# Kernel tuning notes

Measured on AMD Instinct MI355X. Metric: run time of the kernel, lower is better.

## Reference

```python
import jax, jax.numpy as jnp
import numpy as np

DIM = 768
NUM_HEADS = 12
HEAD_DIM = DIM // NUM_HEADS
WS = 14                       # window_size (14, 14)
N_TOK = WS * WS + 1           # 197 (patches + cls)
NUM_REL = (2 * WS - 1) ** 2 + 3  # 732
SCALE = HEAD_DIM ** -0.5


def _build_rel_index():
    # Faithful port of the BEiT relative_position_index construction.
    coords = np.stack(np.meshgrid(np.arange(WS), np.arange(WS), indexing='ij'))  # (2, WS, WS)
    flat = coords.reshape(2, -1)                                   # (2, WS*WS)
    rel = flat[:, :, None] - flat[:, None, :]                      # (2, P, P)
    rel = rel.transpose(1, 2, 0).astype(np.int64)                  # (P, P, 2)
    rel[:, :, 0] += WS - 1
    rel[:, :, 1] += WS - 1
    rel[:, :, 0] *= 2 * WS - 1
    idx = np.zeros((N_TOK, N_TOK), dtype=np.int64)
    idx[1:, 1:] = rel.sum(-1)
    idx[0, :] = NUM_REL - 3
    idx[:, 0] = NUM_REL - 2
    idx[0, 0] = NUM_REL - 1
    return idx


def setup_inputs() -> dict:
    key = jax.random.key(0)
    ks = jax.random.split(key, 7)
    B = 64
    x = jax.random.normal(ks[0], (B, N_TOK, DIM), dtype=jnp.float32)
    qkv_w = jax.random.normal(ks[1], (3 * DIM, DIM), dtype=jnp.float32) * 0.02
    q_bias = jnp.zeros((DIM,), dtype=jnp.float32)
    v_bias = jnp.zeros((DIM,), dtype=jnp.float32)
    rel_table = jax.random.normal(ks[2], (NUM_REL, NUM_HEADS), dtype=jnp.float32) * 0.02
    proj_w = jax.random.normal(ks[3], (DIM, DIM), dtype=jnp.float32) * 0.02
    proj_b = jnp.zeros((DIM,), dtype=jnp.float32)
    rel_index = jnp.asarray(_build_rel_index())  # (N, N) int64
    return {"x": x, "qkv_w": qkv_w, "q_bias": q_bias, "v_bias": v_bias,
            "rel_table": rel_table, "proj_w": proj_w, "proj_b": proj_b,
            "rel_index": rel_index}


def reference(x, qkv_w, q_bias, v_bias, rel_table, proj_w, proj_b, rel_index):
    B, N, C = x.shape
    # qkv bias = concat(q_bias, zeros, v_bias)
    qkv_b = jnp.concatenate([q_bias, jnp.zeros_like(v_bias), v_bias])
    qkv = x @ qkv_w.T + qkv_b                       # (B, N, 3C)
    qkv = qkv.reshape(B, N, 3, NUM_HEADS, HEAD_DIM).transpose(2, 0, 3, 1, 4)
    q, k, v = qkv[0], qkv[1], qkv[2]                # each (B, H, N, hd)
    attn = jnp.einsum('bhqd,bhkd->bhqk', q * SCALE, k)
    # relative position bias gathered from table: (N, N, H) -> (H, N, N)
    bias = rel_table[rel_index].transpose(2, 0, 1)
    attn = attn + bias[None]
    attn = jax.nn.softmax(attn, axis=-1)
    out = jnp.einsum('bhqk,bhkd->bhqd', attn, v)    # (B, H, N, hd)
    out = out.transpose(0, 2, 1, 3).reshape(B, N, -1)
    return out @ proj_w.T + proj_b
```

## Files before the change

### kernel.cpp

```cpp
#include <hip/hip_runtime.h>
#include <stdint.h>

#define NTOK 197
#define HD 64
#define NH 12
#define CDIM 768
#define BB 64
#define MTOT (BB*NTOK)
#define MPAD 12672
#define SCALE 0.125f
#define BTP 208

typedef __attribute__((ext_vector_type(8))) short short8;
typedef __attribute__((ext_vector_type(4))) float f32x4;
typedef unsigned short us;

__device__ __forceinline__ us f2b(float f){
    union { float f; uint32_t u; } v; v.f = f;
    uint32_t u = v.u;
    uint32_t r = u + 0x7fffu + ((u >> 16) & 1u);
    return (us)(r >> 16);
}

__device__ __forceinline__ float b2f(us b){
    union { uint32_t u; float f; } v; v.u = ((uint32_t)b) << 16;
    return v.f;
}

__device__ __forceinline__ void gload16(const us* g, us* l){
    __builtin_amdgcn_global_load_lds((const __attribute__((address_space(1))) void*)g,
                                     (__attribute__((address_space(3))) void*)l, 16, 0, 0);
}

#define LGKM0_BAR() do{ asm volatile("s_waitcnt lgkmcnt(0)" ::: "memory"); \
                        __builtin_amdgcn_s_barrier(); }while(0)

__device__ __forceinline__ void cvt4(const float* in, us* out, int i){
    float4 v = ((const float4*)in)[i];
    ushort4 o;
    o.x = f2b(v.x); o.y = f2b(v.y); o.z = f2b(v.z); o.w = f2b(v.w);
    ((ushort4*)out)[i] = o;
}

__global__ void prep_kernel(const float* __restrict__ x, const float* __restrict__ qkv_w,
                            const float* __restrict__ proj_w,
                            const int* __restrict__ rel_index, const float* __restrict__ rel_table,
                            us* __restrict__ xb, us* __restrict__ wqkv, us* __restrict__ wproj,
                            float* __restrict__ biasT)
{
    const int N1 = MTOT*CDIM/4;
    const int N2 = 3*CDIM*CDIM/4;
    const int N3 = CDIM*CDIM/4;
    const int N4 = BTP*BTP;
    const int total = N1+N2+N3+N4;
    for (int i = blockIdx.x*blockDim.x + threadIdx.x; i < total; i += gridDim.x*blockDim.x){
        if (i < N1) cvt4(x, xb, i);
        else if (i < N1+N2) cvt4(qkv_w, wqkv, i-N1);
        else if (i < N1+N2+N3) cvt4(proj_w, wproj, i-N1-N2);
        else {
            int t = i - N1 - N2 - N3;
            int col = t / BTP, row = t - col*BTP;
            if (row < NTOK && col < NTOK){
                int idx = rel_index[row*NTOK + col];
                #pragma unroll
                for (int h = 0; h < NH; ++h)
                    biasT[((size_t)h*BTP + col)*BTP + row] = rel_table[idx*NH + h];
            } else {
                #pragma unroll
                for (int h = 0; h < NH; ++h)
                    biasT[((size_t)h*BTP + col)*BTP + row] = 0.f;
            }
        }
    }
}

__global__ __launch_bounds__(512,1) void pgemm5_kernel(
    const us* __restrict__ A, const us* __restrict__ Bw,
    us* __restrict__ Qo, us* __restrict__ Ko, us* __restrict__ Vo,
    const float* __restrict__ b0, const float* __restrict__ b2, int ny, int total)
{
    __shared__ __align__(16) us AsB[3][24576];
    us* cbuf = &AsB[2][0];
    const int tid  = threadIdx.x;
    const int lane = tid & 63;
    const int wave = tid >> 6;
    const int wrr = wave >> 2;
    const int wcc = wave & 3;
    const int lr = lane & 15;
    const int g  = lane >> 4;

    const int id  = blockIdx.x;
    const int xcd = id & 7;
    const int jb  = id >> 3;
    const int qs  = total >> 3, rs = total & 7;
    const int Ssp = xcd*qs + (xcd < rs ? xcd : rs);
    const int L   = qs + (xcd < rs ? 1 : 0);
    const int qb  = L >> 5, rb = L & 31;
    const int cnt = qb + (jb < rb ? 1 : 0);
    const int w0  = Ssp + jb*qb + (jb < rb ? jb : rb);
    if (cnt == 0) return;

    int aoff[2], bofs[4];
    int aldo[2], bldo[4];
    #pragma unroll
    for (int p=0;p<2;p++){
        int c = tid + p*512;
        int row = c >> 3, ch = c & 7;
        aoff[p] = row*CDIM + ((ch ^ (row & 7))*8);
        aldo[p] = c*8;
    }
    #pragma unroll
    for (int jj=0;jj<4;jj++){
        int c = tid + jj*512;
        int row = c >> 3, ch = c & 7;
        bofs[jj] = row*CDIM + ((ch ^ (row & 7))*8);
        bldo[jj] = 8192 + c*8;
    }

    const int S = cnt * 12;
    auto stageStep = [&](int x){
        int tt = x / 12, kt = x - tt*12;
        int ww = w0 + tt;
        int bx = ww / ny, by = ww - bx*ny;
        const us* pA = A  + (size_t)(bx*128)*CDIM;
        const us* pB = Bw + (size_t)(by*256)*CDIM;
        int buf = x % 3;
        #pragma unroll
        for (int p=0;p<2;p++) gload16(pA + aoff[p] + kt*64, &AsB[buf][aldo[p]]);
        #pragma unroll
        for (int jj=0;jj<4;jj++) gload16(pB + bofs[jj] + kt*64, &AsB[buf][bldo[jj]]);
    };

    stageStep(0);
    if (S > 1) stageStep(1);
    int s = 0;

    #pragma unroll 1
    for (int tt = 0; tt < cnt; ++tt){
        const int w  = w0 + tt;
        const int bx = w / ny, by = w - bx*ny;
        const int m0 = bx*128, n0 = by*256;
        const int whc = n0 / CDIM;
        float addf[4];
        const float sclf = (whc == 0) ? SCALE : 1.f;
        #pragma unroll
        for (int nt=0;nt<4;nt++){
            int n = n0 + wcc*64 + nt*16 + lr;
            int hn = n - whc*CDIM;
            addf[nt] = (whc == 0) ? b0[hn] : (whc == 2 ? b2[hn] : 0.f);
        }

        f32x4 acc[4][4];
        #pragma unroll
        for (int i=0;i<4;i++)
            #pragma unroll
            for (int jj=0;jj<4;jj++) acc[i][jj] = (f32x4){0.f,0.f,0.f,0.f};

        #pragma unroll 1
        for (int kt = 0; kt < 12; ++kt){
            if (s == S-1) asm volatile("s_waitcnt vmcnt(0)" ::: "memory");
            else          asm volatile("s_waitcnt vmcnt(6)" ::: "memory");
            __builtin_amdgcn_s_barrier();
            if (s + 2 < S) stageStep(s + 2);
            const us* la = &AsB[s % 3][0];
            const us* lb = &AsB[s % 3][8192];
            #pragma unroll
            for (int kk=0; kk<2; ++kk){
                const int co = 8*((kk*4 + g) ^ (lr & 7));
                short8 af[4], bf[4];
                #pragma unroll
                for (int mt=0;mt<4;mt++)
                    af[mt] = *(const short8*)&la[(wrr*64+mt*16+lr)*64 + co];
                #pragma unroll
                for (int nt=0;nt<4;nt++)
                    bf[nt] = *(const short8*)&lb[(wcc*64+nt*16+lr)*64 + co];
                __builtin_amdgcn_s_setprio(1);
                #pragma unroll
                for (int mt=0;mt<4;mt++)
                    #pragma unroll
                    for (int nt=0;nt<4;nt++)
                        acc[mt][nt] = __builtin_amdgcn_mfma_f32_16x16x32_bf16(af[mt], bf[nt], acc[mt][nt], 0,0,0);
                __builtin_amdgcn_s_setprio(0);
            }
            ++s;
        }

        LGKM0_BAR();

        const us* outp = (whc == 0 ? Qo : (whc == 1 ? Ko : Vo));
        #pragma unroll 1
        for (int half = 0; half < 2; ++half){
            if ((wcc >> 1) == half){
                #pragma unroll
                for (int mt=0;mt<4;mt++)
                    #pragma unroll
                    for (int rr=0;rr<4;rr++){
                        int row = wrr*64 + mt*16 + g*4 + rr;
                        #pragma unroll
                        for (int nt=0;nt<4;nt++){
                            int col = (wcc & 1)*64 + nt*16 + lr;
                            cbuf[row*132 + col] = f2b((acc[mt][nt][rr] + addf[nt]) * sclf);
                        }
                    }
            }
            LGKM0_BAR();
            #pragma unroll
            for (int p=0;p<4;p++){
                int c = tid + p*512;
                int row = c >> 4, ch = c & 15;
                int m = m0 + row;
                if (m < MTOT){
                    short8 vv = *(const short8*)&cbuf[row*132 + ch*8];
                    int n = n0 + half*128 + ch*8;
                    int hn = n - whc*CDIM;
                    int h  = hn >> 6, d0 = hn & 63;
                    int bidx = m / NTOK;
                    int tok  = m - bidx*NTOK;
                    size_t off = ((size_t)((bidx*NH + h)*NTOK + tok))*HD + d0;
                    *(short8*)((us*)outp + off) = vv;
                }
            }
            LGKM0_BAR();
        }
    }
}

__global__ __launch_bounds__(256) void proj_gemm_kernel(
    const us* __restrict__ A, const us* __restrict__ Bw,
    float* __restrict__ Cout, const float* __restrict__ b0, int ny)
{
    __shared__ __align__(16) us lds[32768];
    us* As = lds;
    us* Bs = lds + 16384;
    const int tid  = threadIdx.x;
    const int lane = tid & 63;
    const int wave = tid >> 6;
    const int wr = wave >> 1, wc = wave & 1;
    const int lr = lane & 15;
    const int g  = lane >> 4;

    const int NB   = gridDim.x;
    const int base = NB >> 3;
    const int rem  = NB & 7;
    const int id   = blockIdx.x;
    const int xcd  = id & 7;
    const int qq   = id >> 3;
    const int start = (xcd < rem) ? xcd*(base+1) : rem*(base+1) + (xcd-rem)*base;
    const int w    = start + qq;
    const int bx   = w / ny;
    const int by   = w - bx*ny;
    const int m0 = bx * 128;
    const int n0 = by * 128;
    const int NT = CDIM / 128;

    const int row0 = tid >> 4;
    const int cg   = (tid & 15) ^ row0;

    float addf[4];
    #pragma unroll
    for (int nt=0;nt<4;nt++) addf[nt] = b0[n0 + wc*64 + nt*16 + lr];

    f32x4 acc[4][4];
    #pragma unroll
    for (int i=0;i<4;i++)
        #pragma unroll
        for (int j=0;j<4;j++) acc[i][j] = (f32x4){0.f,0.f,0.f,0.f};

    const us* gA = A  + (size_t)(m0 + row0)*CDIM + cg*8;
    const us* gB = Bw + (size_t)(n0 + row0)*CDIM + cg*8;

    #pragma unroll 1
    for (int kt = 0; kt < NT; ++kt){
        __syncthreads();
        #pragma unroll
        for (int j=0;j<8;j++){
            gload16(gA + (size_t)j*16*CDIM + kt*128, As + tid*8 + j*2048);
            gload16(gB + (size_t)j*16*CDIM + kt*128, Bs + tid*8 + j*2048);
        }
        __syncthreads();
        #pragma unroll
        for (int kk=0; kk<4; ++kk){
            const int co = 8*((kk*4 + g) ^ lr);
            short8 af[4], bf[4];
            #pragma unroll
            for (int mt=0;mt<4;mt++)
                af[mt] = *(const short8*)&As[(wr*64+mt*16+lr)*128 + co];
            #pragma unroll
            for (int nt=0;nt<4;nt++)
                bf[nt] = *(const short8*)&Bs[(wc*64+nt*16+lr)*128 + co];
            __builtin_amdgcn_s_setprio(1);
            #pragma unroll
            for (int mt=0;mt<4;mt++)
                #pragma unroll
                for (int nt=0;nt<4;nt++)
                    acc[mt][nt] = __builtin_amdgcn_mfma_f32_16x16x32_bf16(af[mt], bf[nt], acc[mt][nt], 0,0,0);
            __builtin_amdgcn_s_setprio(0);
        }
    }

    __syncthreads();
    #pragma unroll
    for (int mt=0;mt<4;mt++)
        #pragma unroll
        for (int r=0;r<4;r++){
            int row = wr*64 + mt*16 + g*4 + r;
            #pragma unroll
            for (int nt=0;nt<4;nt++){
                int col = wc*64 + nt*16 + lr;
                lds[row*132 + col] = f2b(acc[mt][nt][r] + addf[nt]);
            }
        }
    __syncthreads();
    #pragma unroll
    for (int j=0;j<8;j++){
        int c2  = tid + j*256;
        int row = c2 >> 4;
        int ch  = c2 & 15;
        int m = m0 + row;
        if (m >= MTOT) continue;
        short8 vv = *(const short8*)&lds[row*132 + ch*8];
        int n = n0 + ch*8;
        float4 f0, f1;
        f0.x = b2f((us)vv[0]); f0.y = b2f((us)vv[1]); f0.z = b2f((us)vv[2]); f0.w = b2f((us)vv[3]);
        f1.x = b2f((us)vv[4]); f1.y = b2f((us)vv[5]); f1.z = b2f((us)vv[6]); f1.w = b2f((us)vv[7]);
        *(float4*)&Cout[(size_t)m*CDIM + n]     = f0;
        *(float4*)&Cout[(size_t)m*CDIM + n + 4] = f1;
    }
}

__global__ __launch_bounds__(256) void attn_kernel(
    const us* __restrict__ Q,
    const us* __restrict__ K,
    const us* __restrict__ V,
    const float* __restrict__ biasT,
    us* __restrict__ Ao)
{
    __shared__ us Vt[64][232];
    __shared__ us Ps[4][16][232];
    const int bh = blockIdx.x;
    const int b = bh / NH;
    const int h = bh - b*NH;
    const us* Qh = Q + (size_t)bh*NTOK*HD;
    const us* Kh = K + (size_t)bh*NTOK*HD;
    const us* Vh = V + (size_t)bh*NTOK*HD;
    const float* bT = biasT + (size_t)h*BTP*BTP;
    const int tid = threadIdx.x, lane = tid & 63, wave = tid >> 6;
    const int lr = lane & 15, g = lane >> 4, ko = g*8;

    for (int i = tid; i < 64*232/2; i += 256) ((uint32_t*)Vt)[i] = 0;
    __syncthreads();
    {
        int d0 = (tid & 7) * 8;
        for (int t = tid >> 3; t < NTOK; t += 32){
            short8 v = *(const short8*)&Vh[t*HD + d0];
            #pragma unroll
            for (int j=0;j<8;j++) Vt[d0+j][t] = (us)v[j];
        }
    }
    __syncthreads();

    for (int s = wave; s < 13; s += 4){
        int qrow = s*16 + lr; qrow = qrow > 196 ? 196 : qrow;
        short8 qa0 = *(const short8*)&Qh[qrow*HD + ko];
        short8 qa1 = *(const short8*)&Qh[qrow*HD + 32 + ko];
        f32x4 S[13];
        #pragma unroll
        for (int t=0;t<13;t++){
            int kc = t*16 + lr; kc = kc > 196 ? 196 : kc;
            short8 kb0 = *(const short8*)&Kh[kc*HD + ko];
            short8 kb1 = *(const short8*)&Kh[kc*HD + 32 + ko];
            f32x4 a = (f32x4){0.f,0.f,0.f,0.f};
            a = __builtin_amdgcn_mfma_f32_16x16x32_bf16(qa0, kb0, a, 0,0,0);
            a = __builtin_amdgcn_mfma_f32_16x16x32_bf16(qa1, kb1, a, 0,0,0);
            S[t] = a;
        }
        float rmax[4] = {-3e38f,-3e38f,-3e38f,-3e38f};
        #pragma unroll
        for (int t=0;t<13;t++){
            int col = t*16 + lr;
            bool cok = col < NTOK;
            float4 b4 = *(const float4*)&bT[(size_t)col*BTP + s*16 + g*4];
            #pragma unroll
            for (int r=0;r<4;r++){
                float xv = S[t][r] + ((const float*)&b4)[r];
                xv = cok ? xv : -1e30f;
                S[t][r] = xv;
                rmax[r] = fmaxf(rmax[r], xv);
            }
        }
        #pragma unroll
        for (int r=0;r<4;r++)
            #pragma unroll
            for (int msk=1; msk<16; msk<<=1)
                rmax[r] = fmaxf(rmax[r], __shfl_xor(rmax[r], msk));
        float rsum[4] = {0.f,0.f,0.f,0.f};
        #pragma unroll
        for (int t=0;t<13;t++)
            #pragma unroll
            for (int r=0;r<4;r++){
                float e = __expf(S[t][r] - rmax[r]);
                S[t][r] = e;
                rsum[r] += e;
            }
        #pragma unroll
        for (int r=0;r<4;r++){
            #pragma unroll
            for (int msk=1; msk<16; msk<<=1)
                rsum[r] += __shfl_xor(rsum[r], msk);
            rsum[r] = 1.f / rsum[r];
        }
        #pragma unroll
        for (int t=0;t<13;t++)
            #pragma unroll
            for (int r=0;r<4;r++)
                Ps[wave][g*4+r][t*16+lr] = f2b(S[t][r] * rsum[r]);
        #pragma unroll
        for (int r=0;r<4;r++) Ps[wave][g*4+r][208+lr] = 0;
        asm volatile("s_waitcnt lgkmcnt(0)" ::: "memory");
        f32x4 pv[4];
        #pragma unroll
        for (int nt=0;nt<4;nt++) pv[nt] = (f32x4){0.f,0.f,0.f,0.f};
        #pragma unroll
        for (int ks=0; ks<7; ks++){
            int k0 = ks*32 + ko;
            short8 pa = *(const short8*)&Ps[wave][lr][k0];
            #pragma unroll
            for (int nt=0;nt<4;nt++){
                short8 vb = *(const short8*)&Vt[nt*16+lr][k0];
                pv[nt] = __builtin_amdgcn_mfma_f32_16x16x32_bf16(pa, vb, pv[nt], 0,0,0);
            }
        }
        #pragma unroll
        for (int nt=0;nt<4;nt++)
            #pragma unroll
            for (int r=0;r<4;r++){
                int tok = s*16 + g*4 + r;
                if (tok < NTOK)
                    Ao[(size_t)(b*NTOK + tok)*CDIM + h*HD + nt*16 + lr] = f2b(pv[nt][r]);
            }
    }
}

extern "C" void kernel_launch(void* const* d_in, const int* in_sizes, int n_in,
                              void* d_out, int out_size, void* d_ws, size_t ws_size,
                              hipStream_t stream)
{
    const float* x        = (const float*)d_in[0];
    const float* qkv_w    = (const float*)d_in[1];
    const float* q_bias   = (const float*)d_in[2];
    const float* v_bias   = (const float*)d_in[3];
    const float* rel_tab  = (const float*)d_in[4];
    const float* proj_w   = (const float*)d_in[5];
    const float* proj_b   = (const float*)d_in[6];
    const int*   rel_idx  = (const int*)d_in[7];
    float* out = (float*)d_out;

    char* w = (char*)d_ws;
    us* xb    = (us*)w; w += (size_t)MPAD*CDIM*2;
    us* wqkv  = (us*)w; w += (size_t)3*CDIM*CDIM*2;
    us* wproj = (us*)w; w += (size_t)CDIM*CDIM*2;
    us* Qb    = (us*)w; w += (size_t)BB*NH*NTOK*HD*2;
    us* Kb    = (us*)w; w += (size_t)BB*NH*NTOK*HD*2;
    us* Vb    = (us*)w; w += (size_t)BB*NH*NTOK*HD*2;
    float* biasT = (float*)w; w += (size_t)NH*BTP*BTP*4;
    us* aob   = (us*)w; w += (size_t)MPAD*CDIM*2;

    prep_kernel<<<2048, 256, 0, stream>>>(x, qkv_w, proj_w, rel_idx, rel_tab,
                                          xb, wqkv, wproj, biasT);

    pgemm5_kernel<<<256, 512, 0, stream>>>(xb, wqkv, Qb, Kb, Vb, q_bias, v_bias, 9, 891);
    attn_kernel<<<BB*NH, 256, 0, stream>>>(Qb, Kb, Vb, biasT, aob);
    proj_gemm_kernel<<<594, 256, 0, stream>>>(aob, wproj, out, proj_b, 6);
}
```

Measured before the change: 159.6 us.

## Halve QKV GEMM K-tile to fit two blocks per CU and double grid

The QKV persistent GEMM now stages K in 32-wide chunks instead of 64, which halves the LDS footprint per pipeline buffer. That allows launch_bounds(512,2) and a 512-block grid, with the work split over 64 slots per XCD instead of 32. The swizzle is adapted to 4-chunk rows, and the epilogue is split into four phases so it fits the smaller staging buffer. The aim is better latency hiding through two resident blocks per CU, at the cost of twice as many barriers and wait points per tile and a register cap that may cause spills.

Result: faster. 153.4 us (-3.9%).

```diff
diff --git a/kernel.cpp b/kernel.cpp
--- a/kernel.cpp
+++ b/kernel.cpp
@@ -74,12 +74,12 @@
     }
 }
 
-__global__ __launch_bounds__(512,1) void pgemm5_kernel(
+__global__ __launch_bounds__(512,2) void pgemm6_kernel(
     const us* __restrict__ A, const us* __restrict__ Bw,
     us* __restrict__ Qo, us* __restrict__ Ko, us* __restrict__ Vo,
     const float* __restrict__ b0, const float* __restrict__ b2, int ny, int total)
 {
-    __shared__ __align__(16) us AsB[3][24576];
+    __shared__ __align__(16) us AsB[3][12288];
     us* cbuf = &AsB[2][0];
     const int tid  = threadIdx.x;
     const int lane = tid & 63;
@@ -95,45 +95,44 @@
     const int qs  = total >> 3, rs = total & 7;
     const int Ssp = xcd*qs + (xcd < rs ? xcd : rs);
     const int L   = qs + (xcd < rs ? 1 : 0);
-    const int qb  = L >> 5, rb = L & 31;
+    const int qb  = L >> 6, rb = L & 63;
     const int cnt = qb + (jb < rb ? 1 : 0);
     const int w0  = Ssp + jb*qb + (jb < rb ? jb : rb);
     if (cnt == 0) return;
 
-    int aoff[2], bofs[4];
-    int aldo[2], bldo[4];
+    int aoff, aldo, bofs[2], bldo[2];
+    {
+        int c = tid;
+        int row = c >> 2, ch = c & 3;
+        aoff = row*CDIM + ((ch ^ ((row >> 1) & 3))*8);
+        aldo = c*8;
+    }
     #pragma unroll
-    for (int p=0;p<2;p++){
-        int c = tid + p*512;
-        int row = c >> 3, ch = c & 7;
-        aoff[p] = row*CDIM + ((ch ^ (row & 7))*8);
-        aldo[p] = c*8;
-    }
-    #pragma unroll
-    for (int jj=0;jj<4;jj++){
+    for (int jj=0;jj<2;jj++){
         int c = tid + jj*512;
-        int row = c >> 3, ch = c & 7;
-        bofs[jj] = row*CDIM + ((ch ^ (row & 7))*8);
-        bldo[jj] = 8192 + c*8;
-    }
-
-    const int S = cnt * 12;
+        int row = c >> 2, ch = c & 3;
+        bofs[jj] = row*CDIM + ((ch ^ ((row >> 1) & 3))*8);
+        bldo[jj] = 4096 + c*8;
+    }
+
+    const int S = cnt * 24;
     auto stageStep = [&](int x){
-        int tt = x / 12, kt = x - tt*12;
+        int tt = x / 24, kt = x - tt*24;
         int ww = w0 + tt;
         int bx = ww / ny, by = ww - bx*ny;
         const us* pA = A  + (size_t)(bx*128)*CDIM;
         const us* pB = Bw + (size_t)(by*256)*CDIM;
         int buf = x % 3;
-        #pragma unroll
-        for (int p=0;p<2;p++) gload16(pA + aoff[p] + kt*64, &AsB[buf][aldo[p]]);
-        #pragma unroll
-        for (int jj=0;jj<4;jj++) gload16(pB + bofs[jj] + kt*64, &AsB[buf][bldo[jj]]);
+        gload16(pA + aoff + kt*32, &AsB[buf][aldo]);
+        #pragma unroll
+        for (int jj=0;jj<2;jj++) gload16(pB + bofs[jj] + kt*32, &AsB[buf][bldo[jj]]);
     };
 
     stageStep(0);
     if (S > 1) stageStep(1);
     int s = 0;
+
+    const int co = 8*(g ^ ((lr >> 1) & 3));
 
     #pragma unroll 1
     for (int tt = 0; tt < cnt; ++tt){
@@ -157,31 +156,27 @@
             for (int jj=0;jj<4;jj++) acc[i][jj] = (f32x4){0.f,0.f,0.f,0.f};
 
         #pragma unroll 1
-        for (int kt = 0; kt < 12; ++kt){
+        for (int kt = 0; kt < 24; ++kt){
             if (s == S-1) asm volatile("s_waitcnt vmcnt(0)" ::: "memory");
-            else          asm volatile("s_waitcnt vmcnt(6)" ::: "memory");
+            else          asm volatile("s_waitcnt vmcnt(3)" ::: "memory");
             __builtin_amdgcn_s_barrier();
             if (s + 2 < S) stageStep(s + 2);
             const us* la = &AsB[s % 3][0];
-            const us* lb = &AsB[s % 3][8192];
-            #pragma unroll
-            for (int kk=0; kk<2; ++kk){
-                const int co = 8*((kk*4 + g) ^ (lr & 7));
-                short8 af[4], bf[4];
-                #pragma unroll
-                for (int mt=0;mt<4;mt++)
-                    af[mt] = *(const short8*)&la[(wrr*64+mt*16+lr)*64 + co];
+            const us* lb = &AsB[s % 3][4096];
+            short8 af[4], bf[4];
+            #pragma unroll
+            for (int mt=0;mt<4;mt++)
+                af[mt] = *(const short8*)&la[(wrr*64+mt*16+lr)*32 + co];
+            #pragma unroll
+            for (int nt=0;nt<4;nt++)
+                bf[nt] = *(const short8*)&lb[(wcc*64+nt*16+lr)*32 + co];
+            __builtin_amdgcn_s_setprio(1);
+            #pragma unroll
+            for (int mt=0;mt<4;mt++)
                 #pragma unroll
                 for (int nt=0;nt<4;nt++)
-                    bf[nt] = *(const short8*)&lb[(wcc*64+nt*16+lr)*64 + co];
-                __builtin_amdgcn_s_setprio(1);
-                #pragma unroll
-                for (int mt=0;mt<4;mt++)
-                    #pragma unroll
-                    for (int nt=0;nt<4;nt++)
-                        acc[mt][nt] = __builtin_amdgcn_mfma_f32_16x16x32_bf16(af[mt], bf[nt], acc[mt][nt], 0,0,0);
-                __builtin_amdgcn_s_setprio(0);
-            }
+                    acc[mt][nt] = __builtin_amdgcn_mfma_f32_16x16x32_bf16(af[mt], bf[nt], acc[mt][nt], 0,0,0);
+            __builtin_amdgcn_s_setprio(0);
             ++s;
         }
 
@@ -189,13 +184,15 @@
 
         const us* outp = (whc == 0 ? Qo : (whc == 1 ? Ko : Vo));
         #pragma unroll 1
-        for (int half = 0; half < 2; ++half){
-            if ((wcc >> 1) == half){
+        for (int ph = 0; ph < 4; ++ph){
+            const int half  = ph & 1;
+            const int rhalf = ph >> 1;
+            if (wrr == rhalf && (wcc >> 1) == half){
                 #pragma unroll
                 for (int mt=0;mt<4;mt++)
                     #pragma unroll
                     for (int rr=0;rr<4;rr++){
-                        int row = wrr*64 + mt*16 + g*4 + rr;
+                        int row = mt*16 + g*4 + rr;
                         #pragma unroll
                         for (int nt=0;nt<4;nt++){
                             int col = (wcc & 1)*64 + nt*16 + lr;
@@ -205,10 +202,10 @@
             }
             LGKM0_BAR();
             #pragma unroll
-            for (int p=0;p<4;p++){
+            for (int p=0;p<2;p++){
                 int c = tid + p*512;
                 int row = c >> 4, ch = c & 15;
-                int m = m0 + row;
+                int m = m0 + rhalf*64 + row;
                 if (m < MTOT){
                     short8 vv = *(const short8*)&cbuf[row*132 + ch*8];
                     int n = n0 + half*128 + ch*8;
@@ -468,7 +465,7 @@
     prep_kernel<<<2048, 256, 0, stream>>>(x, qkv_w, proj_w, rel_idx, rel_tab,
                                           xb, wqkv, wproj, biasT);
 
-    pgemm5_kernel<<<256, 512, 0, stream>>>(xb, wqkv, Qb, Kb, Vb, q_bias, v_bias, 9, 891);
+    pgemm6_kernel<<<512, 512, 0, stream>>>(xb, wqkv, Qb, Kb, Vb, q_bias, v_bias, 9, 891);
     attn_kernel<<<BB*NH, 256, 0, stream>>>(Qb, Kb, Vb, biasT, aob);
     proj_gemm_kernel<<<594, 256, 0, stream>>>(aob, wproj, out, proj_b, 6);
 }
```
